# Performance work log

Hardware: AMD Instinct MI355X
Metric: run time of the kernel (lower is better)

Reference implementation:

```python
import jax, jax.numpy as jnp
import numpy as np

V, D, B, L = 8000, 256, 64, 64
CONCENTRATION = 5.0  # config['model']['args']['concentrator_factor']
GAW = 0.5            # initial value of _lambda parameter
EPS_COS = 1e-8       # torch cosine_similarity eps


def setup_inputs() -> dict:
    key = jax.random.key(0)
    ks = jax.random.split(key, 8)
    concepts_list = jax.random.randint(ks[0], (B, L), 0, V)
    concepts_length = jax.random.randint(ks[1], (B,), 0, L)
    contrastive_mask = jax.random.randint(ks[2], (B, V), 0, 2).astype(jnp.int32)
    # raw edge matrix, then row-range normalization as in init_params
    edge_raw = jax.random.uniform(ks[3], (V, V), dtype=jnp.float32)
    rng = (edge_raw.max(axis=1) - edge_raw.min(axis=1))[:, None]
    edge_matrix = edge_raw / (rng + (rng == 0).astype(jnp.float32))
    affectiveness = jax.random.uniform(ks[4], (V,), dtype=jnp.float32)
    embed_w = jax.random.normal(ks[5], (V, D), dtype=jnp.float32)
    embed_kb_w = jax.random.normal(ks[6], (V, D), dtype=jnp.float32)
    lam = jnp.full((V,), GAW, dtype=jnp.float32)
    return {
        "concepts_list": concepts_list,
        "concepts_length": concepts_length,
        "contrastive_mask": contrastive_mask,
        "edge_matrix": edge_matrix,
        "affectiveness": affectiveness,
        "embed_w": embed_w,
        "embed_kb_w": embed_kb_w,
        "lam": lam,
    }


def reference(concepts_list, concepts_length, contrastive_mask,
              edge_matrix, affectiveness, embed_w, embed_kb_w, lam):
    # [B, L, D] concept token embeddings
    concepts_embedded = embed_w[concepts_list]
    # valid-prefix mask per row: positions < concepts_length[i]
    pos_mask = (jnp.arange(L)[None, :] < concepts_length[:, None])  # [B, L] bool
    denom = jnp.maximum(concepts_length, 1).astype(concepts_embedded.dtype)[:, None]
    # per-row masked mean (rows with length 0 -> zeros, matching empty_tensor)
    row_mean = (concepts_embedded * pos_mask[..., None]).sum(axis=1) / denom  # [B, D]
    context_representation = row_mean.mean(axis=0)  # [D]
    # |cosine similarity| between context and every KB embedding -> [V]
    ctx_norm = jnp.linalg.norm(context_representation)
    kb_norms = jnp.linalg.norm(embed_kb_w, axis=1)
    cosine_similarity = jnp.abs(
        (embed_kb_w @ context_representation) / jnp.maximum(kb_norms * ctx_norm, EPS_COS)
    )
    # [B, L, V] local graph rows for each concept token
    local_graph = edge_matrix[concepts_list]
    rel = local_graph * cosine_similarity          # broadcast over V
    aff = (local_graph > 0).astype(local_graph.dtype) * affectiveness
    concepts_weights = lam * rel + (1.0 - lam) * aff  # [B, L, V]
    concepts_weights = jnp.where(contrastive_mask[:, None, :] == 0, 1e-9, concepts_weights)
    attn = jax.nn.softmax(concepts_weights * CONCENTRATION, axis=2)  # [B, L, V]
    concepts_embedding = jnp.einsum('blv,vd->bld', attn, embed_kb_w)  # [B, L, D]
    # masked mean over valid prefix (length 0 -> zeros)
    concepts_embedding = (concepts_embedding * pos_mask[..., None]).sum(axis=1) / denom  # [B, D]
    local_nodes = jnp.broadcast_to(embed_kb_w[None], (B, V, D))
    return concepts_embedding, local_nodes
```

## Files before the change

kernel.cpp:

```cpp
#include <hip/hip_runtime.h>
#include <cstddef>
#include <cstdint>
#include <cmath>

#define V 8000
#define D 256
#define B 64
#define L 64
#define SPLIT 8
#define NB_SM (B * SPLIT)
#define NB_BC 500
#define NCH 200
#define VC 40

#define PART_OFF 0
#define CTX_OFF  16384
#define W1_OFF   16640
#define W0_OFF   24640
#define A_OFF    32640
#define P_OFF    544640

typedef float f32x4 __attribute__((ext_vector_type(4)));

__global__ __launch_bounds__(256) void k1_ctx(const int* __restrict__ clist,
                                              const int* __restrict__ clen,
                                              const float* __restrict__ embw,
                                              float* __restrict__ part) {
    int b = blockIdx.x, d = threadIdx.x;
    __shared__ int cl[L];
    if (d < L) cl[d] = clist[b * L + d];
    __syncthreads();
    int len = clen[b];
    int nl = len < L ? len : L;
    float a0 = 0.f, a1 = 0.f, a2 = 0.f, a3 = 0.f;
    int l = 0;
    for (; l + 4 <= nl; l += 4) {
        a0 += embw[(size_t)cl[l]     * D + d];
        a1 += embw[(size_t)cl[l + 1] * D + d];
        a2 += embw[(size_t)cl[l + 2] * D + d];
        a3 += embw[(size_t)cl[l + 3] * D + d];
    }
    for (; l < nl; ++l) a0 += embw[(size_t)cl[l] * D + d];
    float denom = (float)(len < 1 ? 1 : len);
    part[b * D + d] = (a0 + a1 + a2 + a3) / denom;
}

__global__ void k1b_reduce(const float* __restrict__ part, float* __restrict__ ctx) {
    int d = threadIdx.x;
    float s = 0.f;
    #pragma unroll 8
    for (int b = 0; b < B; ++b) s += part[b * D + d];
    ctx[d] = s * (1.0f / (float)B);
}

__global__ __launch_bounds__(256) void k2_cos(const float* __restrict__ kb,
                                              const float* __restrict__ lam,
                                              const float* __restrict__ aff,
                                              const float* __restrict__ ctx,
                                              float* __restrict__ w1,
                                              float* __restrict__ w0,
                                              float* __restrict__ A) {
    int tid = threadIdx.x;
    int gtid = blockIdx.x * 256 + tid;
    A[gtid] = 0.f;

    __shared__ float ctxs[D];
    __shared__ float red[5];
    int wid = tid >> 6, lane = tid & 63;
    float c = ctx[tid];
    ctxs[tid] = c;
    float sq = c * c;
    #pragma unroll
    for (int o = 32; o > 0; o >>= 1) sq += __shfl_xor(sq, o);
    if (lane == 0) red[wid] = sq;
    __syncthreads();
    if (tid == 0) red[4] = sqrtf(red[0] + red[1] + red[2] + red[3]);
    __syncthreads();
    float ctxnorm = red[4];

    int v = blockIdx.x * 4 + wid;
    float4 k4 = *(const float4*)(kb + (size_t)v * D + lane * 4);
    float4 c4 = *(const float4*)(ctxs + lane * 4);
    float dot = k4.x * c4.x + k4.y * c4.y + k4.z * c4.z + k4.w * c4.w;
    float sqs = k4.x * k4.x + k4.y * k4.y + k4.z * k4.z + k4.w * k4.w;
    #pragma unroll
    for (int o = 32; o > 0; o >>= 1) {
        dot += __shfl_xor(dot, o);
        sqs += __shfl_xor(sqs, o);
    }
    if (lane == 0) {
        float cosv = fabsf(dot) / fmaxf(sqrtf(sqs) * ctxnorm, 1e-8f);
        float la = lam[v];
        w1[v] = 5.0f * la * cosv;
        w0[v] = 5.0f * (1.0f - la) * aff[v];
    }
}

__global__ __launch_bounds__(1024) void k36_fused(
    const int* __restrict__ clist, const int* __restrict__ clen,
    const int* __restrict__ cmask, const float* __restrict__ edge,
    const float* __restrict__ w1g, const float* __restrict__ w0g,
    float* __restrict__ A,
    const f32x4* __restrict__ kb4, f32x4* __restrict__ out4) {
    int g = blockIdx.x;
    int tid = threadIdx.x;

    if (g >= NB_SM) {
        int idx = (g - NB_SM) * 1024 + tid;
        f32x4 f = kb4[idx];
        #pragma unroll
        for (int b = 0; b < B; ++b)
            __builtin_nontemporal_store(f, &out4[(size_t)b * (V * D / 4) + idx]);
        return;
    }

    int b = g >> 3, split = g & (SPLIT - 1);
    int wid = tid >> 6, lane = tid & 63;
    bool active = tid < (V / 8);
    int v0 = tid * 8;
    __shared__ float lsum[2][16];

    float w1r[8], w0r[8], acc[8];
    int mr[8];
    if (active) {
        float4 t0 = *(const float4*)(w1g + v0);
        float4 t1 = *(const float4*)(w1g + v0 + 4);
        w1r[0]=t0.x; w1r[1]=t0.y; w1r[2]=t0.z; w1r[3]=t0.w;
        w1r[4]=t1.x; w1r[5]=t1.y; w1r[6]=t1.z; w1r[7]=t1.w;
        t0 = *(const float4*)(w0g + v0);
        t1 = *(const float4*)(w0g + v0 + 4);
        w0r[0]=t0.x; w0r[1]=t0.y; w0r[2]=t0.z; w0r[3]=t0.w;
        w0r[4]=t1.x; w0r[5]=t1.y; w0r[6]=t1.z; w0r[7]=t1.w;
        int4 m0 = *(const int4*)(cmask + (size_t)b * V + v0);
        int4 m1 = *(const int4*)(cmask + (size_t)b * V + v0 + 4);
        mr[0]=m0.x; mr[1]=m0.y; mr[2]=m0.z; mr[3]=m0.w;
        mr[4]=m1.x; mr[5]=m1.y; mr[6]=m1.z; mr[7]=m1.w;
    }
    #pragma unroll
    for (int j = 0; j < 8; ++j) acc[j] = 0.f;

    int len = clen[b];
    int nl = len < L ? len : L;
    int parity = 0;
    for (int l = split; l < nl; l += SPLIT) {
        int c = clist[b * L + l];
        const float* er = edge + (size_t)c * V;
        float p[8];
        float s = 0.f;
        if (active) {
            float4 e0 = *(const float4*)(er + v0);
            float4 e1 = *(const float4*)(er + v0 + 4);
            float ev[8] = {e0.x, e0.y, e0.z, e0.w, e1.x, e1.y, e1.z, e1.w};
            #pragma unroll
            for (int j = 0; j < 8; ++j) {
                float e = ev[j];
                float wv = w1r[j] * e + (e > 0.f ? w0r[j] : 0.f);
                wv = (mr[j] != 0) ? wv : 5e-9f;
                p[j] = __expf(wv);
                s += p[j];
            }
        } else {
            #pragma unroll
            for (int j = 0; j < 8; ++j) p[j] = 0.f;
        }
        #pragma unroll
        for (int o = 32; o > 0; o >>= 1) s += __shfl_xor(s, o);
        if (lane == 0) lsum[parity][wid] = s;
        __syncthreads();
        float tot = 0.f;
        #pragma unroll
        for (int k = 0; k < 16; ++k) tot += lsum[parity][k];
        float inv = 1.0f / tot;
        if (active) {
            #pragma unroll
            for (int j = 0; j < 8; ++j) acc[j] += p[j] * inv;
        }
        parity ^= 1;
    }
    if (active) {
        #pragma unroll
        for (int j = 0; j < 8; ++j)
            atomicAdd(&A[(size_t)b * V + v0 + j], acc[j]);
    }
}

__global__ __launch_bounds__(256) void k4_gemv(const float* __restrict__ A,
                                               const float* __restrict__ kb,
                                               float* __restrict__ P) {
    int ch = blockIdx.x;
    int tid = threadIdx.x;
    int vbase = ch * VC;
    __shared__ float Al[B][VC];
    for (int i = tid; i < B * VC; i += 256) {
        int bt = i / VC, vl = i % VC;
        Al[bt][vl] = A[(size_t)bt * V + vbase + vl];
    }
    __syncthreads();
    float acc[B];
    #pragma unroll
    for (int t = 0; t < B; ++t) acc[t] = 0.f;
    for (int vl = 0; vl < VC; ++vl) {
        float kv = kb[(size_t)(vbase + vl) * D + tid];
        #pragma unroll
        for (int t = 0; t < B; ++t) acc[t] += Al[t][vl] * kv;
    }
    #pragma unroll
    for (int t = 0; t < B; ++t)
        P[(size_t)ch * (B * D) + (size_t)t * D + tid] = acc[t];
}

__global__ void k5_out0(const float* __restrict__ P, const int* __restrict__ clen,
                        float* __restrict__ out0) {
    int b = blockIdx.x, d = threadIdx.x;
    float s = 0.f;
    #pragma unroll 8
    for (int ch = 0; ch < NCH; ++ch) s += P[(size_t)ch * (B * D) + b * D + d];
    int len = clen[b];
    out0[b * D + d] = s / (float)(len < 1 ? 1 : len);
}

extern "C" void kernel_launch(void* const* d_in, const int* in_sizes, int n_in,
                              void* d_out, int out_size, void* d_ws, size_t ws_size,
                              hipStream_t stream) {
    const int*   clist = (const int*)d_in[0];
    const int*   clen  = (const int*)d_in[1];
    const int*   cmask = (const int*)d_in[2];
    const float* edge  = (const float*)d_in[3];
    const float* aff   = (const float*)d_in[4];
    const float* embw  = (const float*)d_in[5];
    const float* kb    = (const float*)d_in[6];
    const float* lam   = (const float*)d_in[7];
    float* out0 = (float*)d_out;
    float* out1 = out0 + B * D;
    float* ws   = (float*)d_ws;

    k1_ctx<<<dim3(B), dim3(256), 0, stream>>>(clist, clen, embw, ws + PART_OFF);
    k1b_reduce<<<dim3(1), dim3(D), 0, stream>>>(ws + PART_OFF, ws + CTX_OFF);
    k2_cos<<<dim3(V / 4), dim3(256), 0, stream>>>(kb, lam, aff, ws + CTX_OFF,
                                                  ws + W1_OFF, ws + W0_OFF, ws + A_OFF);
    k36_fused<<<dim3(NB_SM + NB_BC), dim3(1024), 0, stream>>>(
        clist, clen, cmask, edge, ws + W1_OFF, ws + W0_OFF, ws + A_OFF,
        (const f32x4*)kb, (f32x4*)out1);
    k4_gemv<<<dim3(NCH), dim3(256), 0, stream>>>(ws + A_OFF, kb, ws + P_OFF);
    k5_out0<<<dim3(B), dim3(D), 0, stream>>>(ws + P_OFF, clen, out0);
}
```

Baseline: 310.8 us.

## Split broadcast copy out of fused softmax kernel into separate launch

The broadcast of the KB embedding table into the [B,V,D] output was fused into the softmax kernel as extra blocks. It now runs as a standalone 256-thread kernel at the end of the stream, where each block copies one contiguous partition with nontemporal stores. This separates a bandwidth-bound copy from the compute-bound softmax so each kernel has uniform blocks, but it gives up the overlap the fused launch allowed and adds a kernel launch.

```diff
diff --git a/kernel.cpp b/kernel.cpp
--- a/kernel.cpp
+++ b/kernel.cpp
@@ -8,10 +8,10 @@
 #define B 64
 #define L 64
 #define SPLIT 8
-#define NB_SM (B * SPLIT)
-#define NB_BC 500
 #define NCH 200
 #define VC 40
+#define NP 25
+#define PSZ (V * D / 4 / NP)
 
 #define PART_OFF 0
 #define CTX_OFF  16384
@@ -96,25 +96,13 @@
     }
 }
 
-__global__ __launch_bounds__(1024) void k36_fused(
+__global__ __launch_bounds__(1024) void k3_softmax(
     const int* __restrict__ clist, const int* __restrict__ clen,
     const int* __restrict__ cmask, const float* __restrict__ edge,
     const float* __restrict__ w1g, const float* __restrict__ w0g,
-    float* __restrict__ A,
-    const f32x4* __restrict__ kb4, f32x4* __restrict__ out4) {
-    int g = blockIdx.x;
+    float* __restrict__ A) {
+    int b = blockIdx.x, split = blockIdx.y;
     int tid = threadIdx.x;
-
-    if (g >= NB_SM) {
-        int idx = (g - NB_SM) * 1024 + tid;
-        f32x4 f = kb4[idx];
-        #pragma unroll
-        for (int b = 0; b < B; ++b)
-            __builtin_nontemporal_store(f, &out4[(size_t)b * (V * D / 4) + idx]);
-        return;
-    }
-
-    int b = g >> 3, split = g & (SPLIT - 1);
     int wid = tid >> 6, lane = tid & 63;
     bool active = tid < (V / 8);
     int v0 = tid * 8;
@@ -219,6 +207,17 @@
     out0[b * D + d] = s / (float)(len < 1 ? 1 : len);
 }
 
+__global__ __launch_bounds__(256) void k6_bcast(const f32x4* __restrict__ kb4,
+                                                f32x4* __restrict__ out4) {
+    int p = blockIdx.x % NP;
+    int b = blockIdx.x / NP;
+    const f32x4* src = kb4 + (size_t)p * PSZ;
+    f32x4* dst = out4 + (size_t)b * (V * D / 4) + (size_t)p * PSZ;
+    #pragma unroll 4
+    for (int i = threadIdx.x; i < PSZ; i += 256)
+        __builtin_nontemporal_store(src[i], &dst[i]);
+}
+
 extern "C" void kernel_launch(void* const* d_in, const int* in_sizes, int n_in,
                               void* d_out, int out_size, void* d_ws, size_t ws_size,
                               hipStream_t stream) {
@@ -238,9 +237,9 @@
     k1b_reduce<<<dim3(1), dim3(D), 0, stream>>>(ws + PART_OFF, ws + CTX_OFF);
     k2_cos<<<dim3(V / 4), dim3(256), 0, stream>>>(kb, lam, aff, ws + CTX_OFF,
                                                   ws + W1_OFF, ws + W0_OFF, ws + A_OFF);
-    k36_fused<<<dim3(NB_SM + NB_BC), dim3(1024), 0, stream>>>(
-        clist, clen, cmask, edge, ws + W1_OFF, ws + W0_OFF, ws + A_OFF,
-        (const f32x4*)kb, (f32x4*)out1);
+    k3_softmax<<<dim3(B, SPLIT), dim3(1024), 0, stream>>>(clist, clen, cmask, edge,
+                                                          ws + W1_OFF, ws + W0_OFF, ws + A_OFF);
     k4_gemv<<<dim3(NCH), dim3(256), 0, stream>>>(ws + A_OFF, kb, ws + P_OFF);
     k5_out0<<<dim3(B), dim3(D), 0, stream>>>(ws + P_OFF, clen, out0);
-}
+    k6_bcast<<<dim3(B * NP), dim3(256), 0, stream>>>((const f32x4*)kb, (f32x4*)out1);
+}
```

New measurement: 346.0 us. +11.3%, slower.
